# Optimization experiments

Hardware: AMD Instinct MI355X
Metric: run time of the kernel (lower is better)

## Reference

```python
import jax, jax.numpy as jnp
import numpy as np


def setup_inputs() -> dict:
    key = jax.random.key(0)
    k0, k1, k2, k3, k4 = jax.random.split(key, 5)
    B, S, H, I, E = 4, 2048, 1024, 3584, 8
    scale = 0.02
    return {
        "hidden_states": jax.random.normal(k0, (B, S, H), jnp.float32),
        "gate_w": jax.random.normal(k1, (E, H), jnp.float32) * scale,
        "Wg": jax.random.normal(k2, (E, I, H), jnp.float32) * scale,
        "Wu": jax.random.normal(k3, (E, I, H), jnp.float32) * scale,
        "Wd": jax.random.normal(k4, (E, H, I), jnp.float32) * scale,
        "top_k": 2,
    }


def reference(hidden_states, gate_w, Wg, Wu, Wd, top_k):
    B, S, H = hidden_states.shape
    E = gate_w.shape[0]
    x = hidden_states.reshape(-1, H)  # [N, H]

    # Router: softmax in float32 (matches torch dtype=torch.float), then top-k + renorm.
    router_logits = x @ gate_w.T  # [N, E]
    routing_probs = jax.nn.softmax(router_logits.astype(jnp.float32), axis=-1)
    top_w, sel = jax.lax.top_k(routing_probs, top_k)  # [N, K]
    top_w = top_w / jnp.sum(top_w, axis=-1, keepdims=True)
    top_w = top_w.astype(x.dtype)

    # Combined per-token weight for each expert: sum of top-k weights routed to it.
    # comb[n, e] = sum_k top_w[n, k] * (sel[n, k] == e)
    comb = jnp.einsum("nk,nke->ne", top_w, jax.nn.one_hot(sel, E, dtype=x.dtype))

    out = jnp.zeros_like(x)
    for e in range(E):  # fixed small loop over experts (structurally distinct weights)
        h = jax.nn.silu(x @ Wg[e].T) * (x @ Wu[e].T)  # [N, I] SwiGLU
        out = out + (h @ Wd[e].T) * comb[:, e:e + 1]
    return out.reshape(B, S, H), router_logits
```

## Files before the change

### kernel.cpp

```cpp
#include <hip/hip_runtime.h>
#include <hip/hip_bf16.h>

#define N_TOK 8192
#define H_DIM 1024
#define I_DIM 3584
#define N_EXP 8
#define N_PAIR (N_TOK * 2)

#define BM 256
#define BN 128
#define BK 32
#define MAX_TILES 72

#define NPAN1 (I_DIM / BN)
#define NPAN2 (H_DIM / BN)
#define NWG1  (MAX_TILES * NPAN1)
#define NWG2  (MAX_TILES * NPAN2 * 2)

typedef short bf16x8 __attribute__((ext_vector_type(8)));
typedef float f32x4 __attribute__((ext_vector_type(4)));

#define CFENCE() asm volatile("" ::: "memory")


#define WS_CNT      0
#define WS_FILL     64
#define WS_OFF      128
#define WS_NTILES   192
#define WS_TILETAB  256
#define WS_SEL      2048
#define WS_WGT      (WS_SEL    + 2 * N_TOK * 4)
#define WS_PTOK     (WS_WGT    + 2 * N_TOK * 4)
#define WS_PW       (WS_PTOK   + N_PAIR * 4)
#define WS_XBF      (WS_PW     + N_PAIR * 4)
#define WS_HBUF     (WS_XBF    + (size_t)N_TOK * H_DIM * 2)
#define WBF_ELEMS   ((size_t)N_EXP * I_DIM * H_DIM)
#define WS_WGBF     (WS_HBUF + (size_t)N_PAIR * I_DIM * 2)
#define WS_WUBF     (WS_WGBF + WBF_ELEMS * 2)
#define WS_END      (WS_WUBF + WBF_ELEMS * 2)

__device__ __forceinline__ unsigned short f2bf(float f) {
  unsigned int u = __float_as_uint(f);
  unsigned int r = (u + 0x7fffu + ((u >> 16) & 1u)) >> 16;
  return (unsigned short)r;
}

__device__ __forceinline__ uint4 pack8(float4 a, float4 b) {
  uint4 r;
  r.x = (unsigned)f2bf(a.x) | ((unsigned)f2bf(a.y) << 16);
  r.y = (unsigned)f2bf(a.z) | ((unsigned)f2bf(a.w) << 16);
  r.z = (unsigned)f2bf(b.x) | ((unsigned)f2bf(b.y) << 16);
  r.w = (unsigned)f2bf(b.z) | ((unsigned)f2bf(b.w) << 16);
  return r;
}

__device__ __forceinline__ void gll16(const ushort* g, ushort* l) {
  __builtin_amdgcn_global_load_lds(
      (const __attribute__((address_space(1))) unsigned int*)g,
      (__attribute__((address_space(3))) unsigned int*)l, 16, 0, 0);
}

__global__ __launch_bounds__(64) void k_router(
    const float* __restrict__ x, const float* __restrict__ gw,
    float* __restrict__ logits, int* __restrict__ sel,
    float* __restrict__ wgt, int* __restrict__ cnt,
    ushort* __restrict__ xbf)
{
  const int n = blockIdx.x;
  const int lane = threadIdx.x;
  const float4* xr = (const float4*)(x + (size_t)n * H_DIM + lane * 16);
  float4 x0 = xr[0], x1 = xr[1], x2 = xr[2], x3 = xr[3];

  uint4* xo = (uint4*)(xbf + (size_t)n * H_DIM + lane * 16);
  xo[0] = pack8(x0, x1);
  xo[1] = pack8(x2, x3);

  float l[N_EXP];
#pragma unroll
  for (int e = 0; e < N_EXP; ++e) {
    const float4* wr = (const float4*)(gw + e * H_DIM + lane * 16);
    float4 w0 = wr[0], w1 = wr[1], w2 = wr[2], w3 = wr[3];
    float p = x0.x * w0.x + x0.y * w0.y + x0.z * w0.z + x0.w * w0.w
            + x1.x * w1.x + x1.y * w1.y + x1.z * w1.z + x1.w * w1.w
            + x2.x * w2.x + x2.y * w2.y + x2.z * w2.z + x2.w * w2.w
            + x3.x * w3.x + x3.y * w3.y + x3.z * w3.z + x3.w * w3.w;
#pragma unroll
    for (int o = 32; o >= 1; o >>= 1) p += __shfl_xor(p, o, 64);
    l[e] = p;
  }
  float m = l[0];
#pragma unroll
  for (int e = 1; e < N_EXP; ++e) m = fmaxf(m, l[e]);
  float pr[N_EXP]; float den = 0.f;
#pragma unroll
  for (int e = 0; e < N_EXP; ++e) { pr[e] = expf(l[e] - m); den += pr[e]; }
#pragma unroll
  for (int e = 0; e < N_EXP; ++e) pr[e] /= den;
  int i0 = 0; float p0 = pr[0];
#pragma unroll
  for (int e = 1; e < N_EXP; ++e) { if (pr[e] > p0) { p0 = pr[e]; i0 = e; } }
  int i1 = -1; float p1 = -1.f;
#pragma unroll
  for (int e = 0; e < N_EXP; ++e) { if (e != i0 && pr[e] > p1) { p1 = pr[e]; i1 = e; } }
  float rs = 1.f / (p0 + p1);
  if (lane == 0) {
    float* lo = logits + (size_t)n * N_EXP;
#pragma unroll
    for (int e = 0; e < N_EXP; ++e) lo[e] = l[e];
    sel[2 * n] = i0; sel[2 * n + 1] = i1;
    wgt[2 * n] = p0 * rs; wgt[2 * n + 1] = p1 * rs;
    atomicAdd(&cnt[i0], 1);
    atomicAdd(&cnt[i1], 1);
  }
}

__global__ void k_prefix(const int* __restrict__ cnt, int* __restrict__ off,
                         int* __restrict__ ntiles, int* __restrict__ tab)
{
  if (threadIdx.x != 0 || blockIdx.x != 0) return;
  int acc = 0, nt = 0;
  for (int e = 0; e < N_EXP; ++e) {
    off[e] = acc;
    int c = cnt[e];
    for (int r = 0; r < c; r += BM) {
      tab[nt * 3 + 0] = e;
      tab[nt * 3 + 1] = acc + r;
      tab[nt * 3 + 2] = (c - r < BM) ? (c - r) : BM;
      nt++;
    }
    acc += c;
  }
  off[N_EXP] = acc;
  *ntiles = nt;
}

__global__ __launch_bounds__(256) void k_scatter(
    const int* __restrict__ sel, const float* __restrict__ wgt,
    const int* __restrict__ off, int* __restrict__ fill,
    int* __restrict__ ptok, float* __restrict__ pw)
{
  int n = blockIdx.x * 256 + threadIdx.x;
  if (n >= N_TOK) return;
#pragma unroll
  for (int k = 0; k < 2; ++k) {
    int e = sel[2 * n + k];
    int pos = atomicAdd(&fill[e], 1);
    int row = off[e] + pos;
    ptok[row] = n;
    pw[row] = wgt[2 * n + k];
  }
}

__global__ __launch_bounds__(256) void k_cvtw(const float* __restrict__ src,
                                              ushort* __restrict__ dst)
{
  size_t i = (size_t)blockIdx.x * 256 + threadIdx.x;
  const float4* s = (const float4*)(src + i * 8);
  float4 a = s[0], b = s[1];
  ((uint4*)dst)[i] = pack8(a, b);
}


__global__ __launch_bounds__(512) void k_mlp1b(
    const ushort* __restrict__ Wg, const ushort* __restrict__ Wu,
    const ushort* __restrict__ xbf, const int* __restrict__ ptok,
    const int* __restrict__ ntiles, const int* __restrict__ tab,
    ushort* __restrict__ hbuf)
{
  __shared__ ushort sA[2][BM * BK];
  __shared__ ushort sG[2][BN * BK];
  __shared__ ushort sU[2][BN * BK];
  __shared__ int stok[BM];

  const int orig = blockIdx.x;
  const int lin = (orig & 7) * (NWG1 >> 3) + (orig >> 3);
  const int tile = lin / NPAN1;
  const int i0 = (lin % NPAN1) * BN;

  if (tile >= *ntiles) return;
  const int e = tab[tile * 3 + 0];
  const int row0 = tab[tile * 3 + 1];
  const int nrows = tab[tile * 3 + 2];
  const int t = threadIdx.x;

  if (t < BM) {
    int tt = t < nrows ? t : (nrows - 1);
    stok[t] = ptok[row0 + tt];
  }
  __syncthreads();

  const int ak = (((t & 3) ^ ((t >> 3) & 3)) * 8);
  const int ar = t >> 2;
  const ushort* ga0 = xbf + (size_t)stok[ar] * H_DIM + ak;
  const ushort* ga1 = xbf + (size_t)stok[128 + ar] * H_DIM + ak;

  const ushort* gg0 = Wg + (size_t)e * I_DIM * H_DIM + (size_t)(i0 + ar) * H_DIM + ak;
  const ushort* gu0 = Wu + (size_t)e * I_DIM * H_DIM + (size_t)(i0 + ar) * H_DIM + ak;

  const int lane = t & 63, wid = t >> 6;
  const int wm = wid >> 1, wn = wid & 1;
  const int fr = lane & 15, fq = lane >> 4;
  const int fs = (fq ^ ((fr >> 1) & 3)) * 8;

  f32x4 ag[4][4], au[4][4];
#pragma unroll
  for (int m = 0; m < 4; ++m)
#pragma unroll
    for (int n = 0; n < 4; ++n) { ag[m][n] = (f32x4){0,0,0,0}; au[m][n] = (f32x4){0,0,0,0}; }

#define STAGE1(b, kt) do {                      \
    gll16(ga0 + (kt), &sA[b][t * 8]);           \
    gll16(ga1 + (kt), &sA[b][(512 + t) * 8]);   \
    gll16(gg0 + (kt), &sG[b][t * 8]);           \
    gll16(gu0 + (kt), &sU[b][t * 8]);           \
  } while (0)

#define COMPUTE1(b) do {                                                     \
    bf16x8 a[4], bg[4], bu[4];                                               \
    _Pragma("unroll")                                                        \
    for (int m = 0; m < 4; ++m)                                              \
      a[m] = *(const bf16x8*)(&sA[b][(wm * 64 + m * 16 + fr) * BK + fs]);    \
    _Pragma("unroll")                                                        \
    for (int n = 0; n < 4; ++n) {                                            \
      bg[n] = *(const bf16x8*)(&sG[b][(wn * 64 + n * 16 + fr) * BK + fs]);   \
      bu[n] = *(const bf16x8*)(&sU[b][(wn * 64 + n * 16 + fr) * BK + fs]);   \
    }                                                                        \
    _Pragma("unroll")                                                        \
    for (int m = 0; m < 4; ++m)                                              \
      _Pragma("unroll")                                                      \
      for (int n = 0; n < 4; ++n) {                                          \
        ag[m][n] = __builtin_amdgcn_mfma_f32_16x16x32_bf16(a[m], bg[n], ag[m][n], 0, 0, 0); \
        au[m][n] = __builtin_amdgcn_mfma_f32_16x16x32_bf16(a[m], bu[n], au[m][n], 0, 0, 0); \
      }                                                                      \
  } while (0)

  const int NK = H_DIM / BK;
  STAGE1(0, 0);
  CFENCE();
  STAGE1(1, BK);
#pragma unroll 2
  for (int ki = 0; ki < NK - 2; ++ki) {
    const int cur = ki & 1;
    asm volatile("s_waitcnt vmcnt(4)" ::: "memory");
    __builtin_amdgcn_s_barrier();
    CFENCE();
    __builtin_amdgcn_sched_barrier(0);
    COMPUTE1(cur);
    asm volatile("s_waitcnt lgkmcnt(0)" ::: "memory");
    __builtin_amdgcn_sched_barrier(0);
    __builtin_amdgcn_s_barrier();
    CFENCE();
    STAGE1(cur, (ki + 2) * BK);
  }
  asm volatile("s_waitcnt vmcnt(4)" ::: "memory");
  __builtin_amdgcn_s_barrier();
  CFENCE();
  __builtin_amdgcn_sched_barrier(0);
  COMPUTE1(0);
  CFENCE();
  asm volatile("s_waitcnt vmcnt(0) lgkmcnt(0)" ::: "memory");
  __builtin_amdgcn_s_barrier();
  CFENCE();
  __builtin_amdgcn_sched_barrier(0);
  COMPUTE1(1);
#undef STAGE1
#undef COMPUTE1

#pragma unroll
  for (int m = 0; m < 4; ++m) {
    const int rb = wm * 64 + m * 16 + fq * 4;
#pragma unroll
    for (int n = 0; n < 4; ++n) {
      const int col = i0 + wn * 64 + n * 16 + fr;
#pragma unroll
      for (int r = 0; r < 4; ++r) {
        const int row = rb + r;
        if (row < nrows) {
          float g = ag[m][n][r], u = au[m][n][r];
          float hv = (g / (1.f + __expf(-g))) * u;
          hbuf[(size_t)(row0 + row) * I_DIM + col] = f2bf(hv);
        }
      }
    }
  }
}

__global__ __launch_bounds__(512) void k_mlp2b(
    const ushort* __restrict__ Wd, const ushort* __restrict__ hbuf,
    const int* __restrict__ ptok, const float* __restrict__ pw,
    const int* __restrict__ ntiles, const int* __restrict__ tab,
    float* __restrict__ out)
{
  __shared__ ushort sA[2][BM * BK];
  __shared__ ushort sB[2][BN * BK];
  __shared__ int stok[BM];
  __shared__ float sw[BM];

  const int orig = blockIdx.x;
  const int lin = (orig & 7) * (NWG2 >> 3) + (orig >> 3);
  const int tile = lin >> 4;
  const int rem = lin & 15;
  const int j0 = (rem >> 1) * BN;
  const int kz = rem & 1;

  if (tile >= *ntiles) return;
  const int e = tab[tile * 3 + 0];
  const int row0 = tab[tile * 3 + 1];
  const int nrows = tab[tile * 3 + 2];
  const int t = threadIdx.x;

  if (t < BM) {
    int tt = t < nrows ? t : (nrows - 1);
    stok[t] = ptok[row0 + tt];
    sw[t] = pw[row0 + tt];
  }
  __syncthreads();

  const int KHALF = I_DIM / 2;
  const int kbase = kz * KHALF;

  const int ak = (((t & 3) ^ ((t >> 3) & 3)) * 8);
  const int ar = t >> 2;
  int arow0 = row0 + ar;        if (arow0 > N_PAIR - 1) arow0 = N_PAIR - 1;
  int arow1 = row0 + 128 + ar;  if (arow1 > N_PAIR - 1) arow1 = N_PAIR - 1;
  const ushort* ga0 = hbuf + (size_t)arow0 * I_DIM + kbase + ak;
  const ushort* ga1 = hbuf + (size_t)arow1 * I_DIM + kbase + ak;

  const ushort* gb0 = Wd + (size_t)e * H_DIM * I_DIM + (size_t)(j0 + ar) * I_DIM + kbase + ak;

  const int lane = t & 63, wid = t >> 6;
  const int wm = wid >> 1, wn = wid & 1;
  const int fr = lane & 15, fq = lane >> 4;
  const int fs = (fq ^ ((fr >> 1) & 3)) * 8;

  f32x4 ac[4][4];
#pragma unroll
  for (int m = 0; m < 4; ++m)
#pragma unroll
    for (int n = 0; n < 4; ++n) ac[m][n] = (f32x4){0,0,0,0};

#define STAGE2(b, kt) do {                      \
    gll16(ga0 + (kt), &sA[b][t * 8]);           \
    gll16(ga1 + (kt), &sA[b][(512 + t) * 8]);   \
    gll16(gb0 + (kt), &sB[b][t * 8]);           \
  } while (0)

#define COMPUTE2(b) do {                                                     \
    bf16x8 a[4], bb[4];                                                      \
    _Pragma("unroll")                                                        \
    for (int m = 0; m < 4; ++m)                                              \
      a[m] = *(const bf16x8*)(&sA[b][(wm * 64 + m * 16 + fr) * BK + fs]);    \
    _Pragma("unroll")                                                        \
    for (int n = 0; n < 4; ++n)                                              \
      bb[n] = *(const bf16x8*)(&sB[b][(wn * 64 + n * 16 + fr) * BK + fs]);   \
    _Pragma("unroll")                                                        \
    for (int m = 0; m < 4; ++m)                                              \
      _Pragma("unroll")                                                      \
      for (int n = 0; n < 4; ++n)                                            \
        ac[m][n] = __builtin_amdgcn_mfma_f32_16x16x32_bf16(a[m], bb[n], ac[m][n], 0, 0, 0); \
  } while (0)

  const int NK = KHALF / BK;
  STAGE2(0, 0);
  CFENCE();
  STAGE2(1, BK);
#pragma unroll 2
  for (int ki = 0; ki < NK - 2; ++ki) {
    const int cur = ki & 1;
    asm volatile("s_waitcnt vmcnt(3)" ::: "memory");
    __builtin_amdgcn_s_barrier();
    CFENCE();
    __builtin_amdgcn_sched_barrier(0);
    COMPUTE2(cur);
    asm volatile("s_waitcnt lgkmcnt(0)" ::: "memory");
    __builtin_amdgcn_sched_barrier(0);
    __builtin_amdgcn_s_barrier();
    CFENCE();
    STAGE2(cur, (ki + 2) * BK);
  }
  asm volatile("s_waitcnt vmcnt(3)" ::: "memory");
  __builtin_amdgcn_s_barrier();
  CFENCE();
  __builtin_amdgcn_sched_barrier(0);
  COMPUTE2(0);
  CFENCE();
  asm volatile("s_waitcnt vmcnt(0) lgkmcnt(0)" ::: "memory");
  __builtin_amdgcn_s_barrier();
  CFENCE();
  __builtin_amdgcn_sched_barrier(0);
  COMPUTE2(1);
#undef STAGE2
#undef COMPUTE2

#pragma unroll
  for (int m = 0; m < 4; ++m) {
    const int rb = wm * 64 + m * 16 + fq * 4;
#pragma unroll
    for (int n = 0; n < 4; ++n) {
      const int col = j0 + wn * 64 + n * 16 + fr;
#pragma unroll
      for (int r = 0; r < 4; ++r) {
        const int row = rb + r;
        if (row < nrows) {
          float v = ac[m][n][r] * sw[row];
          atomicAdd(&out[(size_t)stok[row] * H_DIM + col], v);
        }
      }
    }
  }
}


#define FBM 128
#define FBN 128

__global__ __launch_bounds__(256) void k_mlp1(
    const float* __restrict__ Wg, const float* __restrict__ Wu,
    const ushort* __restrict__ xbf, const int* __restrict__ ptok,
    const int* __restrict__ ntiles, const int* __restrict__ tab,
    ushort* __restrict__ hbuf)
{
  __shared__ ushort sA[FBM * BK];
  __shared__ ushort sG[FBN * BK];
  __shared__ ushort sU[FBN * BK];
  __shared__ int stok[FBM];

  const int tile = blockIdx.x;
  if (tile >= *ntiles) return;
  const int e = tab[tile * 3 + 0];
  const int row0 = tab[tile * 3 + 1] + (blockIdx.z ? FBM : 0);
  int nrows = tab[tile * 3 + 2] - (blockIdx.z ? FBM : 0);
  if (nrows <= 0) return;
  if (nrows > FBM) nrows = FBM;
  const int i0 = blockIdx.y * FBN;
  const int t = threadIdx.x;

  if (t < FBM) {
    int tt = t < nrows ? t : (nrows - 1);
    stok[t] = ptok[row0 + tt];
  }
  __syncthreads();

  const int ak = (t & 3) * 8;
  const ushort* ga0 = xbf + (size_t)stok[t >> 2] * H_DIM + ak;
  const ushort* ga1 = xbf + (size_t)stok[64 + (t >> 2)] * H_DIM + ak;
  ushort* la0 = sA + (size_t)t * 8;
  ushort* la1 = sA + (size_t)(256 + t) * 8;

  const int wr = t >> 1, wcb = (t & 1) * 16;
  const float* gwg = Wg + (size_t)e * I_DIM * H_DIM + (size_t)(i0 + wr) * H_DIM + wcb;
  const float* gwu = Wu + (size_t)e * I_DIM * H_DIM + (size_t)(i0 + wr) * H_DIM + wcb;
  ushort* lwg = sG + wr * BK + wcb;
  ushort* lwu = sU + wr * BK + wcb;

  const int lane = t & 63, wid = t >> 6;
  const int wm = wid >> 1, wn = wid & 1;
  const int fr = lane & 15, fq = lane >> 4;

  f32x4 ag[4][4], au[4][4];
#pragma unroll
  for (int m = 0; m < 4; ++m)
#pragma unroll
    for (int n = 0; n < 4; ++n) { ag[m][n] = (f32x4){0,0,0,0}; au[m][n] = (f32x4){0,0,0,0}; }

  for (int kt = 0; kt < H_DIM; kt += BK) {
    gll16(ga0 + kt, la0);
    gll16(ga1 + kt, la1);

    const float4* pg = (const float4*)(gwg + kt);
    const float4* pu = (const float4*)(gwu + kt);
    float4 g0 = pg[0], g1 = pg[1], g2 = pg[2], g3 = pg[3];
    float4 u0 = pu[0], u1 = pu[1], u2 = pu[2], u3 = pu[3];
    ((uint4*)lwg)[0] = pack8(g0, g1);
    ((uint4*)lwg)[1] = pack8(g2, g3);
    ((uint4*)lwu)[0] = pack8(u0, u1);
    ((uint4*)lwu)[1] = pack8(u2, u3);
    __syncthreads();

    bf16x8 a[4], bg[4], bu[4];
#pragma unroll
    for (int m = 0; m < 4; ++m)
      a[m] = *(const bf16x8*)(sA + (wm * 64 + m * 16 + fr) * BK + fq * 8);
#pragma unroll
    for (int n = 0; n < 4; ++n) {
      bg[n] = *(const bf16x8*)(sG + (wn * 64 + n * 16 + fr) * BK + fq * 8);
      bu[n] = *(const bf16x8*)(sU + (wn * 64 + n * 16 + fr) * BK + fq * 8);
    }
#pragma unroll
    for (int m = 0; m < 4; ++m)
#pragma unroll
      for (int n = 0; n < 4; ++n) {
        ag[m][n] = __builtin_amdgcn_mfma_f32_16x16x32_bf16(a[m], bg[n], ag[m][n], 0, 0, 0);
        au[m][n] = __builtin_amdgcn_mfma_f32_16x16x32_bf16(a[m], bu[n], au[m][n], 0, 0, 0);
      }
    __syncthreads();
  }

#pragma unroll
  for (int m = 0; m < 4; ++m) {
    const int rb = wm * 64 + m * 16 + fq * 4;
#pragma unroll
    for (int n = 0; n < 4; ++n) {
      const int col = i0 + wn * 64 + n * 16 + fr;
#pragma unroll
      for (int r = 0; r < 4; ++r) {
        const int row = rb + r;
        if (row < nrows) {
          float g = ag[m][n][r], u = au[m][n][r];
          float hv = (g / (1.f + __expf(-g))) * u;
          hbuf[(size_t)(row0 + row) * I_DIM + col] = f2bf(hv);
        }
      }
    }
  }
}

__global__ __launch_bounds__(256) void k_mlp2(
    const float* __restrict__ Wd, const ushort* __restrict__ hbuf,
    const int* __restrict__ ptok, const float* __restrict__ pw,
    const int* __restrict__ ntiles, const int* __restrict__ tab,
    float* __restrict__ out)
{
  __shared__ ushort sA[FBM * BK];
  __shared__ ushort sB[FBN * BK];
  __shared__ int stok[FBM];
  __shared__ float sw[FBM];

  const int tile = blockIdx.x;
  if (tile >= *ntiles) return;
  const int e = tab[tile * 3 + 0];
  const int row0 = tab[tile * 3 + 1] + (blockIdx.z ? FBM : 0);
  int nrows = tab[tile * 3 + 2] - (blockIdx.z ? FBM : 0);
  if (nrows <= 0) return;
  if (nrows > FBM) nrows = FBM;
  const int j0 = blockIdx.y * FBN;
  const int t = threadIdx.x;

  if (t < FBM) {
    int tt = t < nrows ? t : (nrows - 1);
    stok[t] = ptok[row0 + tt];
    sw[t] = pw[row0 + tt];
  }
  __syncthreads();

  const int ak = (t & 3) * 8;
  int arow0 = row0 + (t >> 2);       if (arow0 > N_PAIR - 1) arow0 = N_PAIR - 1;
  int arow1 = row0 + 64 + (t >> 2);  if (arow1 > N_PAIR - 1) arow1 = N_PAIR - 1;
  const ushort* ga0 = hbuf + (size_t)arow0 * I_DIM + ak;
  const ushort* ga1 = hbuf + (size_t)arow1 * I_DIM + ak;
  ushort* la0 = sA + (size_t)t * 8;
  ushort* la1 = sA + (size_t)(256 + t) * 8;

  const int wr = t >> 1, wcb = (t & 1) * 16;
  const float* gb = Wd + (size_t)e * H_DIM * I_DIM + (size_t)(j0 + wr) * I_DIM + wcb;
  ushort* lb = sB + wr * BK + wcb;

  const int lane = t & 63, wid = t >> 6;
  const int wm = wid >> 1, wn = wid & 1;
  const int fr = lane & 15, fq = lane >> 4;

  f32x4 ac[4][4];
#pragma unroll
  for (int m = 0; m < 4; ++m)
#pragma unroll
    for (int n = 0; n < 4; ++n) ac[m][n] = (f32x4){0,0,0,0};

  for (int kt = 0; kt < I_DIM; kt += BK) {
    gll16(ga0 + kt, la0);
    gll16(ga1 + kt, la1);

    const float4* pb = (const float4*)(gb + kt);
    float4 b0 = pb[0], b1 = pb[1], b2 = pb[2], b3 = pb[3];
    ((uint4*)lb)[0] = pack8(b0, b1);
    ((uint4*)lb)[1] = pack8(b2, b3);
    __syncthreads();

    bf16x8 a[4], bb[4];
#pragma unroll
    for (int m = 0; m < 4; ++m)
      a[m] = *(const bf16x8*)(sA + (wm * 64 + m * 16 + fr) * BK + fq * 8);
#pragma unroll
    for (int n = 0; n < 4; ++n)
      bb[n] = *(const bf16x8*)(sB + (wn * 64 + n * 16 + fr) * BK + fq * 8);
#pragma unroll
    for (int m = 0; m < 4; ++m)
#pragma unroll
      for (int n = 0; n < 4; ++n)
        ac[m][n] = __builtin_amdgcn_mfma_f32_16x16x32_bf16(a[m], bb[n], ac[m][n], 0, 0, 0);
    __syncthreads();
  }

#pragma unroll
  for (int m = 0; m < 4; ++m) {
    const int rb = wm * 64 + m * 16 + fq * 4;
#pragma unroll
    for (int n = 0; n < 4; ++n) {
      const int col = j0 + wn * 64 + n * 16 + fr;
#pragma unroll
      for (int r = 0; r < 4; ++r) {
        const int row = rb + r;
        if (row < nrows) {
          float v = ac[m][n][r] * sw[row];
          atomicAdd(&out[(size_t)stok[row] * H_DIM + col], v);
        }
      }
    }
  }
}

extern "C" void kernel_launch(void* const* d_in, const int* in_sizes, int n_in,
                              void* d_out, int out_size, void* d_ws, size_t ws_size,
                              hipStream_t stream)
{
  const float* x  = (const float*)d_in[0];
  const float* gw = (const float*)d_in[1];
  const float* Wg = (const float*)d_in[2];
  const float* Wu = (const float*)d_in[3];
  const float* Wd = (const float*)d_in[4];

  float* out    = (float*)d_out;
  float* logits = out + (size_t)N_TOK * H_DIM;

  char* ws = (char*)d_ws;
  int*    cnt    = (int*)(ws + WS_CNT);
  int*    fill   = (int*)(ws + WS_FILL);
  int*    off    = (int*)(ws + WS_OFF);
  int*    ntiles = (int*)(ws + WS_NTILES);
  int*    tab    = (int*)(ws + WS_TILETAB);
  int*    sel    = (int*)(ws + WS_SEL);
  float*  wgt    = (float*)(ws + WS_WGT);
  int*    ptok   = (int*)(ws + WS_PTOK);
  float*  pw     = (float*)(ws + WS_PW);
  ushort* xbf    = (ushort*)(ws + WS_XBF);
  ushort* hbuf   = (ushort*)(ws + WS_HBUF);
  ushort* wgbf   = (ushort*)(ws + WS_WGBF);
  ushort* wubf   = (ushort*)(ws + WS_WUBF);
  ushort* wdbf   = wgbf;

  const bool fast = (ws_size >= WS_END);

  hipMemsetAsync(d_out, 0, (size_t)N_TOK * H_DIM * sizeof(float), stream);
  hipMemsetAsync(ws, 0, 128, stream);

  k_router<<<N_TOK, 64, 0, stream>>>(x, gw, logits, sel, wgt, cnt, xbf);
  k_prefix<<<1, 64, 0, stream>>>(cnt, off, ntiles, tab);
  k_scatter<<<N_TOK / 256, 256, 0, stream>>>(sel, wgt, off, fill, ptok, pw);

  const int cvtblocks = (int)(WBF_ELEMS / 8 / 256);

  if (fast) {
    k_cvtw<<<cvtblocks, 256, 0, stream>>>(Wg, wgbf);
    k_cvtw<<<cvtblocks, 256, 0, stream>>>(Wu, wubf);
    k_mlp1b<<<NWG1, 512, 0, stream>>>(wgbf, wubf, xbf, ptok, ntiles, tab, hbuf);
    k_cvtw<<<cvtblocks, 256, 0, stream>>>(Wd, wdbf);
    k_mlp2b<<<NWG2, 512, 0, stream>>>(wdbf, hbuf, ptok, pw, ntiles, tab, out);
  } else {
    dim3 gA(MAX_TILES, I_DIM / FBN, 2);
    dim3 gB(MAX_TILES, H_DIM / FBN, 2);
    k_mlp1<<<gA, 256, 0, stream>>>(Wg, Wu, xbf, ptok, ntiles, tab, hbuf);
    k_mlp2<<<gB, 256, 0, stream>>>(Wd, hbuf, ptok, pw, ntiles, tab, out);
  }
}
```

Before: 959.0 us.

## Replace atomic scatter-add with per-pair output buffer and deterministic reduce

The down-projection no longer splits K in two with atomic accumulation into the output. Each pair row now writes its weighted result into an fp32 per-pair buffer, and a new reduce kernel sums each token's two rows, which removes the output memset and the atomics. Both GEMM kernels also remap block indices so groups of tiles share a weight panel, aiming for better L2 reuse. The cost is an extra 64MB write plus read and one more launch, and the K-split removal halves the down-projection grid. The new path depends on a larger workspace being available.

Result: faster. 918.8 us (-4.2%).

```diff
diff --git a/kernel.cpp b/kernel.cpp
--- a/kernel.cpp
+++ b/kernel.cpp
@@ -14,14 +14,16 @@
 
 #define NPAN1 (I_DIM / BN)
 #define NPAN2 (H_DIM / BN)
+#define TG1   4
+#define TG2   2
 #define NWG1  (MAX_TILES * NPAN1)
-#define NWG2  (MAX_TILES * NPAN2 * 2)
+#define NWG2  (MAX_TILES * NPAN2)
 
 typedef short bf16x8 __attribute__((ext_vector_type(8)));
 typedef float f32x4 __attribute__((ext_vector_type(4)));
 
 #define CFENCE() asm volatile("" ::: "memory")
-
+#define MFMA_BF16 __builtin_amdgcn_mfma_f32_16x16x32_bf16
 
 #define WS_CNT      0
 #define WS_FILL     64
@@ -38,6 +40,9 @@
 #define WS_WGBF     (WS_HBUF + (size_t)N_PAIR * I_DIM * 2)
 #define WS_WUBF     (WS_WGBF + WBF_ELEMS * 2)
 #define WS_END      (WS_WUBF + WBF_ELEMS * 2)
+#define WS_TOKROW   WS_END
+#define WS_OBUF     (WS_TOKROW + (size_t)2 * N_TOK * 4)
+#define WS_END2     (WS_OBUF + (size_t)N_PAIR * H_DIM * 4)
 
 __device__ __forceinline__ unsigned short f2bf(float f) {
   unsigned int u = __float_as_uint(f);
@@ -137,7 +142,8 @@
 __global__ __launch_bounds__(256) void k_scatter(
     const int* __restrict__ sel, const float* __restrict__ wgt,
     const int* __restrict__ off, int* __restrict__ fill,
-    int* __restrict__ ptok, float* __restrict__ pw)
+    int* __restrict__ ptok, float* __restrict__ pw,
+    int* __restrict__ tokrow)
 {
   int n = blockIdx.x * 256 + threadIdx.x;
   if (n >= N_TOK) return;
@@ -148,6 +154,7 @@
     int row = off[e] + pos;
     ptok[row] = n;
     pw[row] = wgt[2 * n + k];
+    if (tokrow) tokrow[2 * n + k] = row;
   }
 }
 
@@ -158,6 +165,21 @@
   const float4* s = (const float4*)(src + i * 8);
   float4 a = s[0], b = s[1];
   ((uint4*)dst)[i] = pack8(a, b);
+}
+
+__global__ __launch_bounds__(256) void k_reduce(
+    const float* __restrict__ obuf, const int* __restrict__ tokrow,
+    float* __restrict__ out)
+{
+  const int n = blockIdx.x;
+  const int t = threadIdx.x;
+  const int r0 = tokrow[2 * n];
+  const int r1 = tokrow[2 * n + 1];
+  const float4* p0 = (const float4*)(obuf + (size_t)r0 * H_DIM);
+  const float4* p1 = (const float4*)(obuf + (size_t)r1 * H_DIM);
+  float4 a = p0[t], b = p1[t];
+  float4 v = make_float4(a.x + b.x, a.y + b.y, a.z + b.z, a.w + b.w);
+  ((float4*)(out + (size_t)n * H_DIM))[t] = v;
 }
 
 
@@ -174,8 +196,10 @@
 
   const int orig = blockIdx.x;
   const int lin = (orig & 7) * (NWG1 >> 3) + (orig >> 3);
-  const int tile = lin / NPAN1;
-  const int i0 = (lin % NPAN1) * BN;
+  const int grp = lin / (NPAN1 * TG1);
+  const int rem = lin % (NPAN1 * TG1);
+  const int tile = grp * TG1 + (rem % TG1);
+  const int i0 = (rem / TG1) * BN;
 
   if (tile >= *ntiles) return;
   const int e = tab[tile * 3 + 0];
@@ -193,7 +217,6 @@
   const int ar = t >> 2;
   const ushort* ga0 = xbf + (size_t)stok[ar] * H_DIM + ak;
   const ushort* ga1 = xbf + (size_t)stok[128 + ar] * H_DIM + ak;
-
   const ushort* gg0 = Wg + (size_t)e * I_DIM * H_DIM + (size_t)(i0 + ar) * H_DIM + ak;
   const ushort* gu0 = Wu + (size_t)e * I_DIM * H_DIM + (size_t)(i0 + ar) * H_DIM + ak;
 
@@ -229,8 +252,8 @@
     for (int m = 0; m < 4; ++m)                                              \
       _Pragma("unroll")                                                      \
       for (int n = 0; n < 4; ++n) {                                          \
-        ag[m][n] = __builtin_amdgcn_mfma_f32_16x16x32_bf16(a[m], bg[n], ag[m][n], 0, 0, 0); \
-        au[m][n] = __builtin_amdgcn_mfma_f32_16x16x32_bf16(a[m], bu[n], au[m][n], 0, 0, 0); \
+        ag[m][n] = MFMA_BF16(a[m], bg[n], ag[m][n], 0, 0, 0);                \
+        au[m][n] = MFMA_BF16(a[m], bu[n], au[m][n], 0, 0, 0);                \
       }                                                                      \
   } while (0)
 
@@ -285,11 +308,12 @@
   }
 }
 
+template <int EPI>
 __global__ __launch_bounds__(512) void k_mlp2b(
     const ushort* __restrict__ Wd, const ushort* __restrict__ hbuf,
     const int* __restrict__ ptok, const float* __restrict__ pw,
     const int* __restrict__ ntiles, const int* __restrict__ tab,
-    float* __restrict__ out)
+    float* __restrict__ dst)
 {
   __shared__ ushort sA[2][BM * BK];
   __shared__ ushort sB[2][BN * BK];
@@ -298,10 +322,10 @@
 
   const int orig = blockIdx.x;
   const int lin = (orig & 7) * (NWG2 >> 3) + (orig >> 3);
-  const int tile = lin >> 4;
-  const int rem = lin & 15;
-  const int j0 = (rem >> 1) * BN;
-  const int kz = rem & 1;
+  const int grp = lin / (NPAN2 * TG2);
+  const int rem = lin % (NPAN2 * TG2);
+  const int tile = grp * TG2 + (rem % TG2);
+  const int j0 = (rem / TG2) * BN;
 
   if (tile >= *ntiles) return;
   const int e = tab[tile * 3 + 0];
@@ -316,17 +340,13 @@
   }
   __syncthreads();
 
-  const int KHALF = I_DIM / 2;
-  const int kbase = kz * KHALF;
-
   const int ak = (((t & 3) ^ ((t >> 3) & 3)) * 8);
   const int ar = t >> 2;
   int arow0 = row0 + ar;        if (arow0 > N_PAIR - 1) arow0 = N_PAIR - 1;
   int arow1 = row0 + 128 + ar;  if (arow1 > N_PAIR - 1) arow1 = N_PAIR - 1;
-  const ushort* ga0 = hbuf + (size_t)arow0 * I_DIM + kbase + ak;
-  const ushort* ga1 = hbuf + (size_t)arow1 * I_DIM + kbase + ak;
-
-  const ushort* gb0 = Wd + (size_t)e * H_DIM * I_DIM + (size_t)(j0 + ar) * I_DIM + kbase + ak;
+  const ushort* ga0 = hbuf + (size_t)arow0 * I_DIM + ak;
+  const ushort* ga1 = hbuf + (size_t)arow1 * I_DIM + ak;
+  const ushort* gb0 = Wd + (size_t)e * H_DIM * I_DIM + (size_t)(j0 + ar) * I_DIM + ak;
 
   const int lane = t & 63, wid = t >> 6;
   const int wm = wid >> 1, wn = wid & 1;
@@ -357,10 +377,10 @@
     for (int m = 0; m < 4; ++m)                                              \
       _Pragma("unroll")                                                      \
       for (int n = 0; n < 4; ++n)                                            \
-        ac[m][n] = __builtin_amdgcn_mfma_f32_16x16x32_bf16(a[m], bb[n], ac[m][n], 0, 0, 0); \
+        ac[m][n] = MFMA_BF16(a[m], bb[n], ac[m][n], 0, 0, 0);                \
   } while (0)
 
-  const int NK = KHALF / BK;
+  const int NK = I_DIM / BK;
   STAGE2(0, 0);
   CFENCE();
   STAGE2(1, BK);
@@ -403,7 +423,11 @@
         const int row = rb + r;
         if (row < nrows) {
           float v = ac[m][n][r] * sw[row];
-          atomicAdd(&out[(size_t)stok[row] * H_DIM + col], v);
+          if (EPI == 0) {
+            dst[(size_t)(row0 + row) * H_DIM + col] = v;
+          } else {
+            atomicAdd(&dst[(size_t)stok[row] * H_DIM + col], v);
+          }
         }
       }
     }
@@ -490,8 +514,8 @@
     for (int m = 0; m < 4; ++m)
 #pragma unroll
       for (int n = 0; n < 4; ++n) {
-        ag[m][n] = __builtin_amdgcn_mfma_f32_16x16x32_bf16(a[m], bg[n], ag[m][n], 0, 0, 0);
-        au[m][n] = __builtin_amdgcn_mfma_f32_16x16x32_bf16(a[m], bu[n], au[m][n], 0, 0, 0);
+        ag[m][n] = MFMA_BF16(a[m], bg[n], ag[m][n], 0, 0, 0);
+        au[m][n] = MFMA_BF16(a[m], bu[n], au[m][n], 0, 0, 0);
       }
     __syncthreads();
   }
@@ -586,7 +610,7 @@
     for (int m = 0; m < 4; ++m)
 #pragma unroll
       for (int n = 0; n < 4; ++n)
-        ac[m][n] = __builtin_amdgcn_mfma_f32_16x16x32_bf16(a[m], bb[n], ac[m][n], 0, 0, 0);
+        ac[m][n] = MFMA_BF16(a[m], bb[n], ac[m][n], 0, 0, 0);
     __syncthreads();
   }
 
@@ -636,15 +660,20 @@
   ushort* wgbf   = (ushort*)(ws + WS_WGBF);
   ushort* wubf   = (ushort*)(ws + WS_WUBF);
   ushort* wdbf   = wgbf;
-
-  const bool fast = (ws_size >= WS_END);
-
-  hipMemsetAsync(d_out, 0, (size_t)N_TOK * H_DIM * sizeof(float), stream);
+  int*    tokrow = (int*)(ws + WS_TOKROW);
+  float*  obuf   = (float*)(ws + WS_OBUF);
+
+  const bool fast  = (ws_size >= WS_END);
+  const bool fast2 = (ws_size >= WS_END2);
+
+  if (!(fast && fast2))
+    hipMemsetAsync(d_out, 0, (size_t)N_TOK * H_DIM * sizeof(float), stream);
   hipMemsetAsync(ws, 0, 128, stream);
 
   k_router<<<N_TOK, 64, 0, stream>>>(x, gw, logits, sel, wgt, cnt, xbf);
   k_prefix<<<1, 64, 0, stream>>>(cnt, off, ntiles, tab);
-  k_scatter<<<N_TOK / 256, 256, 0, stream>>>(sel, wgt, off, fill, ptok, pw);
+  k_scatter<<<N_TOK / 256, 256, 0, stream>>>(sel, wgt, off, fill, ptok, pw,
+                                             fast2 ? tokrow : (int*)nullptr);
 
   const int cvtblocks = (int)(WBF_ELEMS / 8 / 256);
 
@@ -653,7 +682,12 @@
     k_cvtw<<<cvtblocks, 256, 0, stream>>>(Wu, wubf);
     k_mlp1b<<<NWG1, 512, 0, stream>>>(wgbf, wubf, xbf, ptok, ntiles, tab, hbuf);
     k_cvtw<<<cvtblocks, 256, 0, stream>>>(Wd, wdbf);
-    k_mlp2b<<<NWG2, 512, 0, stream>>>(wdbf, hbuf, ptok, pw, ntiles, tab, out);
+    if (fast2) {
+      k_mlp2b<0><<<NWG2, 512, 0, stream>>>(wdbf, hbuf, ptok, pw, ntiles, tab, obuf);
+      k_reduce<<<N_TOK, 256, 0, stream>>>(obuf, tokrow, out);
+    } else {
+      k_mlp2b<1><<<NWG2, 512, 0, stream>>>(wdbf, hbuf, ptok, pw, ntiles, tab, out);
+    }
   } else {
     dim3 gA(MAX_TILES, I_DIM / FBN, 2);
     dim3 gB(MAX_TILES, H_DIM / FBN, 2);
```
